# Performance work log

Measured on AMD Instinct MI355X. Metric: run time of the kernel, lower is better.

The kernel has to match this reference:

```python
import jax, jax.numpy as jnp
import numpy as np

N_NODES = 100000
N_EDGES = 1600000
D_FEAT = 128
HIDDEN = 256


def setup_inputs() -> dict:
    key = jax.random.key(0)
    k1, k2, k3, k4, k5, k6, k7 = jax.random.split(key, 7)
    h = jax.random.normal(k1, (N_NODES, D_FEAT), dtype=jnp.float32)
    src = jax.random.randint(k2, (N_EDGES,), 0, N_NODES, dtype=jnp.int64)
    dst = jax.random.randint(k3, (N_EDGES,), 0, N_NODES, dtype=jnp.int64)
    # Linear weights, torch layout: W [out, in], b [out]
    lim1 = 1.0 / np.sqrt(2 * D_FEAT)
    W1_w = jax.random.uniform(k4, (HIDDEN, 2 * D_FEAT), minval=-lim1, maxval=lim1, dtype=jnp.float32)
    W1_b = jax.random.uniform(k5, (HIDDEN,), minval=-lim1, maxval=lim1, dtype=jnp.float32)
    lim2 = 1.0 / np.sqrt(HIDDEN)
    W2_w = jax.random.uniform(k6, (1, HIDDEN), minval=-lim2, maxval=lim2, dtype=jnp.float32)
    W2_b = jax.random.uniform(k7, (1,), minval=-lim2, maxval=lim2, dtype=jnp.float32)
    return {"h": h, "src": src, "dst": dst, "W1_w": W1_w, "W1_b": W1_b, "W2_w": W2_w, "W2_b": W2_b}


def reference(h, src, dst, W1_w, W1_b, W2_w, W2_b):
    # gather per-edge src/dst node features and concat: [E, 2D]
    x = jnp.concatenate([h[src], h[dst]], axis=1)
    # Linear -> ReLU -> Linear, squeeze last dim -> [E]
    hid = jax.nn.relu(x @ W1_w.T + W1_b)          # [E, H]
    score = (hid @ W2_w.T + W2_b)[:, 0]           # [E]
    return score
```

## Files before the change

### kernel.cpp

```cpp
#include <hip/hip_runtime.h>


#define NNODES 100000
#define E_TOTAL 1600000
#define D 128
#define K2 256
#define H 256

typedef short bf16x8 __attribute__((ext_vector_type(8)));
typedef float f32x4 __attribute__((ext_vector_type(4)));
typedef const __attribute__((address_space(1))) unsigned short* gas_t;
typedef __attribute__((address_space(3))) unsigned short* las_t;

__device__ __forceinline__ unsigned short f2bf(float f) {
    unsigned u = __float_as_uint(f);
    u += 0x7fff + ((u >> 16) & 1);
    return (unsigned short)(u >> 16);
}
__device__ __forceinline__ float bf2f(unsigned short s) {
    return __uint_as_float((unsigned)s << 16);
}

__global__ void cvt_kernel(const float* __restrict__ h, const float* __restrict__ w1,
                           unsigned short* __restrict__ hbf, unsigned short* __restrict__ w1bf,
                           int n4h, int n4w) {
    int i = blockIdx.x * blockDim.x + threadIdx.x;
    const float* s; unsigned short* d; int j;
    if (i < n4h) { s = h; d = hbf; j = i; }
    else if (i < n4h + n4w) { s = w1; d = w1bf; j = i - n4h; }
    else return;
    float4 v = ((const float4*)s)[j];
    ushort4 o;
    o.x = f2bf(v.x); o.y = f2bf(v.y); o.z = f2bf(v.z); o.w = f2bf(v.w);
    ((ushort4*)d)[j] = o;
}

__global__ __launch_bounds__(256, 4) void u_gemm3(
    const unsigned short* __restrict__ hbf,
    const unsigned short* __restrict__ w1bf,
    const float* __restrict__ b1,
    unsigned short* __restrict__ Us,
    unsigned short* __restrict__ Ud)
{
    __shared__ __align__(16) unsigned short A[64 * 128];

    const int tid = threadIdx.x;
    const int wave = tid >> 6;
    const int lane = tid & 63;
    const int l15 = lane & 15;
    const int quad = lane >> 4;

    const int tile = blockIdx.x >> 2;
    const int half = (blockIdx.x >> 1) & 1;
    const int nh = blockIdx.x & 1;
    const int r0 = tile * 64;
    int rows = NNODES - r0; if (rows > 64) rows = 64;
    const int koff = half * 128;
    unsigned short* U = half ? Ud : Us;

#pragma unroll
    for (int it = 0; it < 4; ++it) {
        const int s = it * 256 + tid;
        const int r = s >> 4;
        const int p = s & 15;
        const int c = p ^ (r & 15);
        if (r < rows)
            __builtin_amdgcn_global_load_lds(
                (gas_t)(hbf + (size_t)(r0 + r) * D + c * 8),
                (las_t)(A + it * 2048 + wave * 512), 16, 0, 0);
    }

    bf16x8 B[4][2];
    float bias[2];
#pragma unroll
    for (int nt = 0; nt < 2; ++nt) {
        const int n = nh * 128 + wave * 32 + nt * 16 + l15;
        bias[nt] = half ? 0.f : b1[n];
#pragma unroll
        for (int kit = 0; kit < 4; ++kit)
            B[kit][nt] = *(const bf16x8*)(w1bf + (size_t)n * K2 + koff + kit * 32 + quad * 8);
    }

    __syncthreads();

    f32x4 acc[4][2];
    const f32x4 zero = {0.f, 0.f, 0.f, 0.f};
#pragma unroll
    for (int ms = 0; ms < 4; ++ms)
#pragma unroll
        for (int nt = 0; nt < 2; ++nt)
            acc[ms][nt] = zero;

#pragma unroll
    for (int kit = 0; kit < 4; ++kit) {
        bf16x8 a[4];
#pragma unroll
        for (int ms = 0; ms < 4; ++ms) {
            const int row = ms * 16 + l15;
            const int p = (kit * 4 + quad) ^ l15;
            a[ms] = *(const bf16x8*)&A[row * 128 + p * 8];
        }
#pragma unroll
        for (int ms = 0; ms < 4; ++ms)
#pragma unroll
            for (int nt = 0; nt < 2; ++nt)
                acc[ms][nt] = __builtin_amdgcn_mfma_f32_16x16x32_bf16(
                    a[ms], B[kit][nt], acc[ms][nt], 0, 0, 0);
    }

    const int coff = nh * 128 + wave * 32 + l15 * 2;
#pragma unroll
    for (int ms = 0; ms < 4; ++ms) {
#pragma unroll
        for (int r = 0; r < 4; ++r) {
            const int m = ms * 16 + quad * 4 + r;
            if (m < rows) {
                const unsigned lo = f2bf(acc[ms][0][r] + bias[0]);
                const unsigned hi = f2bf(acc[ms][1][r] + bias[1]);
                *(unsigned*)(U + (size_t)(r0 + m) * H + coff) = lo | (hi << 16);
            }
        }
    }
}

__global__ __launch_bounds__(256) void edge_score(
    const unsigned short* __restrict__ Us,
    const unsigned short* __restrict__ Ud,
    const int* __restrict__ srcE,
    const int* __restrict__ dstE,
    const float* __restrict__ w2,
    const float* __restrict__ b2p,
    float* __restrict__ out)
{
    const int gt = blockIdx.x * 256 + threadIdx.x;
    const int l = gt & 15;
    const int q = gt >> 4;
    const int Q = (gridDim.x * 256) >> 4;
    const int NGRP = E_TOTAL / 4;

    float w2v[16];
#pragma unroll
    for (int j = 0; j < 16; ++j) {
        const int cp = l * 16 + j;
        const int n = (cp & ~31) + ((cp & 1) << 4) + ((cp & 31) >> 1);
        w2v[j] = w2[n];
    }
    const float b2 = *b2p;

    for (int g = q; g < NGRP; g += Q) {
        const int e0 = g * 4;
        const int4 s4 = *(const int4*)(srcE + e0);
        const int4 d4 = *(const int4*)(dstE + e0);
        const int sv[4] = {s4.x, s4.y, s4.z, s4.w};
        const int dv[4] = {d4.x, d4.y, d4.z, d4.w};

        bf16x8 u[4][2], v[4][2];
#pragma unroll
        for (int k = 0; k < 4; ++k) {
            const bf16x8* us = (const bf16x8*)(Us + (size_t)sv[k] * H + l * 16);
            const bf16x8* ud = (const bf16x8*)(Ud + (size_t)dv[k] * H + l * 16);
            u[k][0] = us[0]; u[k][1] = us[1];
            v[k][0] = ud[0]; v[k][1] = ud[1];
        }

        float4 res;
        float* resp = (float*)&res;
#pragma unroll
        for (int k = 0; k < 4; ++k) {
            float acc = 0.f;
#pragma unroll
            for (int j = 0; j < 8; ++j) {
                float hv = bf2f((unsigned short)u[k][0][j]) + bf2f((unsigned short)v[k][0][j]);
                acc = fmaf(fmaxf(hv, 0.f), w2v[j], acc);
            }
#pragma unroll
            for (int j = 0; j < 8; ++j) {
                float hv = bf2f((unsigned short)u[k][1][j]) + bf2f((unsigned short)v[k][1][j]);
                acc = fmaf(fmaxf(hv, 0.f), w2v[j + 8], acc);
            }
            acc += __shfl_xor(acc, 1, 16);
            acc += __shfl_xor(acc, 2, 16);
            acc += __shfl_xor(acc, 4, 16);
            acc += __shfl_xor(acc, 8, 16);
            resp[k] = acc + b2;
        }
        if (l == 0) *(float4*)(out + e0) = res;
    }
}


#define TILE_M 32
#define NTILES (E_TOTAL / TILE_M)
#define GRID 2500

#if defined(__has_attribute)
#if __has_attribute(amdgpu_waves_per_eu)
#define LB __launch_bounds__(256) __attribute__((amdgpu_waves_per_eu(2, 2)))
#else
#define LB __launch_bounds__(256, 2)
#endif
#else
#define LB __launch_bounds__(256, 2)
#endif

__global__ LB void edge_mlp(
    const unsigned short* __restrict__ hbf,
    const int* __restrict__ srcE,
    const int* __restrict__ dstE,
    const unsigned short* __restrict__ w1bf,
    const float* __restrict__ b1,
    const float* __restrict__ w2,
    const float* __restrict__ b2p,
    float* __restrict__ out)
{
    __shared__ __align__(16) unsigned short X[2][TILE_M * K2];
    __shared__ float red[2][TILE_M][5];

    const int tid = threadIdx.x;
    const int wave = tid >> 6;
    const int lane = tid & 63;
    const int lane15 = lane & 15;
    const int quad = lane >> 4;

    bf16x8 B[8][4];
#pragma unroll
    for (int kit = 0; kit < 8; ++kit)
#pragma unroll
        for (int nt = 0; nt < 4; ++nt) {
            int n = wave * 64 + nt * 16 + lane15;
            int k = kit * 32 + quad * 8;
            B[kit][nt] = *(const bf16x8*)(w1bf + n * K2 + k);
        }

    float b1v[4], w2v[4];
#pragma unroll
    for (int nt = 0; nt < 4; ++nt) {
        int n = wave * 64 + nt * 16 + lane15;
        b1v[nt] = b1[n];
        w2v[nt] = w2[n];
    }
    const float b2 = *b2p;

    const int r_off = tid >> 5;
    const int c = (tid & 31) ^ (r_off & 7);
    const int half = c >> 4;
    const int fc = c & 15;
    const int* idx_base = half ? dstE : srcE;
    const int gshort = fc * 8;

    const int t0 = blockIdx.x;
    int inode[4];

#pragma unroll
    for (int it = 0; it < 4; ++it)
        inode[it] = idx_base[t0 * TILE_M + it * 8 + r_off];
#pragma unroll
    for (int it = 0; it < 4; ++it)
        __builtin_amdgcn_global_load_lds(
            (gas_t)(hbf + inode[it] * D + gshort),
            (las_t)(&X[0][0] + it * 2048 + wave * 512), 16, 0, 0);
    {
        const int t1 = t0 + GRID;
#pragma unroll
        for (int it = 0; it < 4; ++it)
            inode[it] = idx_base[t1 * TILE_M + it * 8 + r_off];
    }

    int buf = 0;
    int prev_eb = -1;

    for (int tile = t0; tile < NTILES; tile += GRID) {
        __syncthreads();

        const int nt1 = tile + GRID;
        if (nt1 < NTILES) {
            unsigned short* Xn = &X[buf ^ 1][0];
#pragma unroll
            for (int it = 0; it < 4; ++it)
                __builtin_amdgcn_global_load_lds(
                    (gas_t)(hbf + inode[it] * D + gshort),
                    (las_t)(Xn + it * 2048 + wave * 512), 16, 0, 0);
        }
        const int nt2 = tile + 2 * GRID;
        if (nt2 < NTILES) {
            const int eb2 = nt2 * TILE_M;
#pragma unroll
            for (int it = 0; it < 4; ++it)
                inode[it] = idx_base[eb2 + it * 8 + r_off];
        }
        if (prev_eb >= 0 && tid < TILE_M) {
            float s = b2;
#pragma unroll
            for (int w = 0; w < 4; ++w) s += red[buf ^ 1][tid][w];
            out[prev_eb + tid] = s;
        }

        const unsigned short* Xc = &X[buf][0];
        f32x4 acc[2][4];
        const f32x4 zero = {0.f, 0.f, 0.f, 0.f};
#pragma unroll
        for (int ms = 0; ms < 2; ++ms)
#pragma unroll
            for (int nt = 0; nt < 4; ++nt)
                acc[ms][nt] = zero;

#pragma unroll
        for (int kit = 0; kit < 8; ++kit) {
            const int p8 = (((kit * 4 + quad) ^ (lane15 & 7))) * 8;
            bf16x8 a[2];
#pragma unroll
            for (int ms = 0; ms < 2; ++ms)
                a[ms] = *(const bf16x8*)&Xc[(ms * 16 + lane15) * K2 + p8];
#pragma unroll
            for (int ms = 0; ms < 2; ++ms)
#pragma unroll
                for (int nt = 0; nt < 4; ++nt)
                    acc[ms][nt] = __builtin_amdgcn_mfma_f32_16x16x32_bf16(
                        a[ms], B[kit][nt], acc[ms][nt], 0, 0, 0);
        }

#pragma unroll
        for (int ms = 0; ms < 2; ++ms)
#pragma unroll
            for (int r = 0; r < 4; ++r) {
                float p = 0.f;
#pragma unroll
                for (int nt = 0; nt < 4; ++nt) {
                    float hv = acc[ms][nt][r] + b1v[nt];
                    p = fmaf(fmaxf(hv, 0.f), w2v[nt], p);
                }
                p += __shfl_xor(p, 1, 16);
                p += __shfl_xor(p, 2, 16);
                p += __shfl_xor(p, 4, 16);
                p += __shfl_xor(p, 8, 16);
                if (lane15 == 0) red[buf][ms * 16 + quad * 4 + r][wave] = p;
            }
        prev_eb = tile * TILE_M;
        buf ^= 1;
    }

    __syncthreads();
    if (prev_eb >= 0 && tid < TILE_M) {
        float s = b2;
#pragma unroll
        for (int w = 0; w < 4; ++w) s += red[buf ^ 1][tid][w];
        out[prev_eb + tid] = s;
    }
}


extern "C" void kernel_launch(void* const* d_in, const int* in_sizes, int n_in,
                              void* d_out, int out_size, void* d_ws, size_t ws_size,
                              hipStream_t stream) {
    const float* h    = (const float*)d_in[0];
    const int*   srcE = (const int*)d_in[1];
    const int*   dstE = (const int*)d_in[2];
    const float* W1   = (const float*)d_in[3];
    const float* b1   = (const float*)d_in[4];
    const float* w2   = (const float*)d_in[5];
    const float* b2   = (const float*)d_in[6];
    float* out = (float*)d_out;

    char* ws = (char*)d_ws;
    const size_t offUs   = 0;
    const size_t offUd   = 51200000;
    const size_t offHbf  = 102400000;
    const size_t offW1bf = 128000000;
    const size_t need    = offW1bf + 131072;

    if (ws_size >= need) {
        unsigned short* Us   = (unsigned short*)(ws + offUs);
        unsigned short* Ud   = (unsigned short*)(ws + offUd);
        unsigned short* hbf  = (unsigned short*)(ws + offHbf);
        unsigned short* w1bf = (unsigned short*)(ws + offW1bf);

        int n4h = NNODES * D / 4, n4w = H * K2 / 4;
        cvt_kernel<<<(n4h + n4w + 255) / 256, 256, 0, stream>>>(h, W1, hbf, w1bf, n4h, n4w);
        u_gemm3<<<4 * ((NNODES + 63) / 64), 256, 0, stream>>>(hbf, w1bf, b1, Us, Ud);
        edge_score<<<4096, 256, 0, stream>>>(Us, Ud, srcE, dstE, w2, b2, out);
    } else {
        unsigned short* hbf  = (unsigned short*)d_ws;
        unsigned short* w1bf = hbf + (size_t)NNODES * D;
        int n4h = NNODES * D / 4, n4w = H * K2 / 4;
        cvt_kernel<<<(n4h + n4w + 255) / 256, 256, 0, stream>>>(h, W1, hbf, w1bf, n4h, n4w);
        edge_mlp<<<GRID, 256, 0, stream>>>(hbf, srcE, dstE, w1bf, b1, w2, b2, out);
    }
}
```

Measured before the change: 359.7 us.

## Split edge scoring into two half-hidden passes to shrink gathered working set

The edge-scoring kernel now runs twice, each pass gathering only 128 of the 256 hidden columns from the per-node Us/Ud tables. The second pass reads back and accumulates the partial result written by the first. The intent is to halve the random-gather footprint per pass so more of each half-table stays resident in cache. In exchange it adds an extra launch, a second read of the edge index arrays, and a read-modify-write of the output.

```diff
diff --git a/kernel.cpp b/kernel.cpp
--- a/kernel.cpp
+++ b/kernel.cpp
@@ -123,14 +123,15 @@
     }
 }
 
-__global__ __launch_bounds__(256) void edge_score(
+__global__ __launch_bounds__(256) void edge_score_half(
     const unsigned short* __restrict__ Us,
     const unsigned short* __restrict__ Ud,
     const int* __restrict__ srcE,
     const int* __restrict__ dstE,
     const float* __restrict__ w2,
     const float* __restrict__ b2p,
-    float* __restrict__ out)
+    float* __restrict__ out,
+    int half)
 {
     const int gt = blockIdx.x * 256 + threadIdx.x;
     const int l = gt & 15;
@@ -138,14 +139,15 @@
     const int Q = (gridDim.x * 256) >> 4;
     const int NGRP = E_TOTAL / 4;
 
-    float w2v[16];
-#pragma unroll
-    for (int j = 0; j < 16; ++j) {
-        const int cp = l * 16 + j;
+    float w2v[8];
+#pragma unroll
+    for (int j = 0; j < 8; ++j) {
+        const int cp = half * 128 + l * 8 + j;
         const int n = (cp & ~31) + ((cp & 1) << 4) + ((cp & 31) >> 1);
         w2v[j] = w2[n];
     }
     const float b2 = *b2p;
+    const int loff = half * 128 + l * 8;
 
     for (int g = q; g < NGRP; g += Q) {
         const int e0 = g * 4;
@@ -154,35 +156,32 @@
         const int sv[4] = {s4.x, s4.y, s4.z, s4.w};
         const int dv[4] = {d4.x, d4.y, d4.z, d4.w};
 
-        bf16x8 u[4][2], v[4][2];
+        bf16x8 u[4], v[4];
 #pragma unroll
         for (int k = 0; k < 4; ++k) {
-            const bf16x8* us = (const bf16x8*)(Us + (size_t)sv[k] * H + l * 16);
-            const bf16x8* ud = (const bf16x8*)(Ud + (size_t)dv[k] * H + l * 16);
-            u[k][0] = us[0]; u[k][1] = us[1];
-            v[k][0] = ud[0]; v[k][1] = ud[1];
-        }
+            u[k] = *(const bf16x8*)(Us + (size_t)sv[k] * H + loff);
+            v[k] = *(const bf16x8*)(Ud + (size_t)dv[k] * H + loff);
+        }
+
+        float4 prev;
+        if (half) prev = *(const float4*)(out + e0);
 
         float4 res;
         float* resp = (float*)&res;
+        const float* prevp = (const float*)&prev;
 #pragma unroll
         for (int k = 0; k < 4; ++k) {
             float acc = 0.f;
 #pragma unroll
             for (int j = 0; j < 8; ++j) {
-                float hv = bf2f((unsigned short)u[k][0][j]) + bf2f((unsigned short)v[k][0][j]);
+                float hv = bf2f((unsigned short)u[k][j]) + bf2f((unsigned short)v[k][j]);
                 acc = fmaf(fmaxf(hv, 0.f), w2v[j], acc);
-            }
-#pragma unroll
-            for (int j = 0; j < 8; ++j) {
-                float hv = bf2f((unsigned short)u[k][1][j]) + bf2f((unsigned short)v[k][1][j]);
-                acc = fmaf(fmaxf(hv, 0.f), w2v[j + 8], acc);
             }
             acc += __shfl_xor(acc, 1, 16);
             acc += __shfl_xor(acc, 2, 16);
             acc += __shfl_xor(acc, 4, 16);
             acc += __shfl_xor(acc, 8, 16);
-            resp[k] = acc + b2;
+            resp[k] = acc + (half ? prevp[k] : b2);
         }
         if (l == 0) *(float4*)(out + e0) = res;
     }
@@ -377,7 +376,8 @@
         int n4h = NNODES * D / 4, n4w = H * K2 / 4;
         cvt_kernel<<<(n4h + n4w + 255) / 256, 256, 0, stream>>>(h, W1, hbf, w1bf, n4h, n4w);
         u_gemm3<<<4 * ((NNODES + 63) / 64), 256, 0, stream>>>(hbf, w1bf, b1, Us, Ud);
-        edge_score<<<4096, 256, 0, stream>>>(Us, Ud, srcE, dstE, w2, b2, out);
+        edge_score_half<<<4096, 256, 0, stream>>>(Us, Ud, srcE, dstE, w2, b2, out, 0);
+        edge_score_half<<<4096, 256, 0, stream>>>(Us, Ud, srcE, dstE, w2, b2, out, 1);
     } else {
         unsigned short* hbf  = (unsigned short*)d_ws;
         unsigned short* w1bf = hbf + (size_t)NNODES * D;
```

Result: no change. 363.7 us (+1.1%).

## Bucket-sort edges by source node block before per-edge gather scoring

Applied to the files above, without the earlier changes.

Adds a counting sort of edges into 64-node source buckets: the histogram is fused into the GEMM kernel, followed by a single-block scan and an atomic scatter. The scoring kernel then walks the sorted edges, so Us rows are gathered with better locality, and it writes each result back to the edge's original index. XCD-aware block remapping is also applied to both the GEMM and the scoring grid to improve L2 locality per chiplet. The cost is two extra launches, atomic scatter traffic, extra index arrays and scattered output writes.

```diff
diff --git a/kernel.cpp b/kernel.cpp
--- a/kernel.cpp
+++ b/kernel.cpp
@@ -6,6 +6,8 @@
 #define D 128
 #define K2 256
 #define H 256
+#define NBUCK ((NNODES + 63) >> 6)
+#define EDGE_GRID 3125
 
 typedef short bf16x8 __attribute__((ext_vector_type(8)));
 typedef float f32x4 __attribute__((ext_vector_type(4)));
@@ -21,14 +23,24 @@
     return __uint_as_float((unsigned)s << 16);
 }
 
+__device__ __forceinline__ int xcd_chunk(int orig, int nwg) {
+    const int q = nwg >> 3, r = nwg & 7;
+    const int x = orig & 7, s = orig >> 3;
+    return (x < r ? x * (q + 1) : r * (q + 1) + (x - r) * q) + s;
+}
+
 __global__ void cvt_kernel(const float* __restrict__ h, const float* __restrict__ w1,
                            unsigned short* __restrict__ hbf, unsigned short* __restrict__ w1bf,
-                           int n4h, int n4w) {
+                           int n4h, int n4w, int* __restrict__ hist, int nz) {
     int i = blockIdx.x * blockDim.x + threadIdx.x;
+    if (i >= n4h + n4w) {
+        int z = i - (n4h + n4w);
+        if (z < nz) hist[z] = 0;
+        return;
+    }
     const float* s; unsigned short* d; int j;
     if (i < n4h) { s = h; d = hbf; j = i; }
-    else if (i < n4h + n4w) { s = w1; d = w1bf; j = i - n4h; }
-    else return;
+    else { s = w1; d = w1bf; j = i - n4h; }
     float4 v = ((const float4*)s)[j];
     ushort4 o;
     o.x = f2bf(v.x); o.y = f2bf(v.y); o.z = f2bf(v.z); o.w = f2bf(v.w);
@@ -40,7 +52,9 @@
     const unsigned short* __restrict__ w1bf,
     const float* __restrict__ b1,
     unsigned short* __restrict__ Us,
-    unsigned short* __restrict__ Ud)
+    unsigned short* __restrict__ Ud,
+    const int* __restrict__ srcE,
+    int* __restrict__ hist)
 {
     __shared__ __align__(16) unsigned short A[64 * 128];
 
@@ -50,9 +64,10 @@
     const int l15 = lane & 15;
     const int quad = lane >> 4;
 
-    const int tile = blockIdx.x >> 2;
-    const int half = (blockIdx.x >> 1) & 1;
-    const int nh = blockIdx.x & 1;
+    const int L = xcd_chunk(blockIdx.x, gridDim.x);
+    const int tile = L >> 2;
+    const int half = (L >> 1) & 1;
+    const int nh = L & 1;
     const int r0 = tile * 64;
     int rows = NNODES - r0; if (rows > 64) rows = 64;
     const int koff = half * 128;
@@ -70,6 +85,11 @@
                 (las_t)(A + it * 2048 + wave * 512), 16, 0, 0);
     }
 
+    if (hist) {
+        const int gid = blockIdx.x * 256 + tid;
+        if (gid < E_TOTAL) atomicAdd(&hist[srcE[gid] >> 6], 1);
+    }
+
     bf16x8 B[4][2];
     float bias[2];
 #pragma unroll
@@ -119,6 +139,117 @@
                 const unsigned hi = f2bf(acc[ms][1][r] + bias[1]);
                 *(unsigned*)(U + (size_t)(r0 + m) * H + coff) = lo | (hi << 16);
             }
+        }
+    }
+}
+
+__global__ void scan_kernel(const int* __restrict__ hist, int* __restrict__ cursor) {
+    __shared__ int tsum[256];
+    const int t = threadIdx.x;
+    int loc[7];
+    int s = 0;
+#pragma unroll
+    for (int j = 0; j < 7; ++j) {
+        const int idx = t * 7 + j;
+        const int v = (idx < NBUCK) ? hist[idx] : 0;
+        loc[j] = s; s += v;
+    }
+    tsum[t] = s;
+    __syncthreads();
+    for (int off = 1; off < 256; off <<= 1) {
+        const int v = (t >= off) ? tsum[t - off] : 0;
+        __syncthreads();
+        tsum[t] += v;
+        __syncthreads();
+    }
+    const int excl = tsum[t] - s;
+#pragma unroll
+    for (int j = 0; j < 7; ++j) {
+        const int idx = t * 7 + j;
+        if (idx < NBUCK) cursor[idx] = excl + loc[j];
+    }
+}
+
+__global__ __launch_bounds__(256) void scatter_kernel(
+    const int* __restrict__ srcE, const int* __restrict__ dstE,
+    int* __restrict__ cursor,
+    int* __restrict__ ss, int* __restrict__ sd, int* __restrict__ si)
+{
+    const int e = blockIdx.x * 256 + threadIdx.x;
+    const int s = srcE[e];
+    const int d = dstE[e];
+    const int p = atomicAdd(&cursor[s >> 6], 1);
+    ss[p] = s; sd[p] = d; si[p] = e;
+}
+
+__global__ __launch_bounds__(256) void edge_score_sorted(
+    const unsigned short* __restrict__ Us,
+    const unsigned short* __restrict__ Ud,
+    const int* __restrict__ ss,
+    const int* __restrict__ sd,
+    const int* __restrict__ si,
+    const float* __restrict__ w2,
+    const float* __restrict__ b2p,
+    float* __restrict__ out)
+{
+    const int b = xcd_chunk(blockIdx.x, gridDim.x);
+    const int tid = threadIdx.x;
+    const int l = tid & 15;
+    const int grp = b * 16 + (tid >> 4);
+
+    float w2v[16];
+#pragma unroll
+    for (int j = 0; j < 16; ++j) {
+        const int cp = l * 16 + j;
+        const int n = (cp & ~31) + ((cp & 1) << 4) + ((cp & 31) >> 1);
+        w2v[j] = w2[n];
+    }
+    const float b2 = *b2p;
+
+    const int g0 = grp * 8;
+    for (int g = g0; g < g0 + 8; ++g) {
+        const int e0 = g * 4;
+        const int4 s4 = *(const int4*)(ss + e0);
+        const int4 d4 = *(const int4*)(sd + e0);
+        const int4 i4 = *(const int4*)(si + e0);
+        const int sv[4] = {s4.x, s4.y, s4.z, s4.w};
+        const int dv[4] = {d4.x, d4.y, d4.z, d4.w};
+
+        bf16x8 u[4][2], v[4][2];
+#pragma unroll
+        for (int k = 0; k < 4; ++k) {
+            const bf16x8* us = (const bf16x8*)(Us + (size_t)sv[k] * H + l * 16);
+            const bf16x8* ud = (const bf16x8*)(Ud + (size_t)dv[k] * H + l * 16);
+            u[k][0] = us[0]; u[k][1] = us[1];
+            v[k][0] = ud[0]; v[k][1] = ud[1];
+        }
+
+        float4 res;
+        float* resp = (float*)&res;
+#pragma unroll
+        for (int k = 0; k < 4; ++k) {
+            float acc = 0.f;
+#pragma unroll
+            for (int j = 0; j < 8; ++j) {
+                float hv = bf2f((unsigned short)u[k][0][j]) + bf2f((unsigned short)v[k][0][j]);
+                acc = fmaf(fmaxf(hv, 0.f), w2v[j], acc);
+            }
+#pragma unroll
+            for (int j = 0; j < 8; ++j) {
+                float hv = bf2f((unsigned short)u[k][1][j]) + bf2f((unsigned short)v[k][1][j]);
+                acc = fmaf(fmaxf(hv, 0.f), w2v[j + 8], acc);
+            }
+            acc += __shfl_xor(acc, 1, 16);
+            acc += __shfl_xor(acc, 2, 16);
+            acc += __shfl_xor(acc, 4, 16);
+            acc += __shfl_xor(acc, 8, 16);
+            resp[k] = acc + b2;
+        }
+        if (l == 0) {
+            out[i4.x] = res.x;
+            out[i4.y] = res.y;
+            out[i4.z] = res.z;
+            out[i4.w] = res.w;
         }
     }
 }
@@ -367,22 +498,44 @@
     const size_t offHbf  = 102400000;
     const size_t offW1bf = 128000000;
     const size_t need    = offW1bf + 131072;
+    const size_t offHist = need;
+    const size_t offCur  = offHist + 8192;
+    const size_t offSS   = offCur + 8192;
+    const size_t offSD   = offSS + 6400000;
+    const size_t offSI   = offSD + 6400000;
+    const size_t need2   = offSI + 6400000;
 
     if (ws_size >= need) {
         unsigned short* Us   = (unsigned short*)(ws + offUs);
         unsigned short* Ud   = (unsigned short*)(ws + offUd);
         unsigned short* hbf  = (unsigned short*)(ws + offHbf);
         unsigned short* w1bf = (unsigned short*)(ws + offW1bf);
+        const bool sorted = (ws_size >= need2);
+        int* hist = sorted ? (int*)(ws + offHist) : (int*)nullptr;
+        int* cur  = (int*)(ws + offCur);
+        int* ss   = (int*)(ws + offSS);
+        int* sd   = (int*)(ws + offSD);
+        int* si   = (int*)(ws + offSI);
 
         int n4h = NNODES * D / 4, n4w = H * K2 / 4;
-        cvt_kernel<<<(n4h + n4w + 255) / 256, 256, 0, stream>>>(h, W1, hbf, w1bf, n4h, n4w);
-        u_gemm3<<<4 * ((NNODES + 63) / 64), 256, 0, stream>>>(hbf, w1bf, b1, Us, Ud);
-        edge_score<<<4096, 256, 0, stream>>>(Us, Ud, srcE, dstE, w2, b2, out);
+        const int nz = sorted ? NBUCK : 0;
+        cvt_kernel<<<(n4h + n4w + nz + 255) / 256, 256, 0, stream>>>(
+            h, W1, hbf, w1bf, n4h, n4w, hist, nz);
+        u_gemm3<<<4 * ((NNODES + 63) / 64), 256, 0, stream>>>(
+            hbf, w1bf, b1, Us, Ud, srcE, hist);
+        if (sorted) {
+            scan_kernel<<<1, 256, 0, stream>>>(hist, cur);
+            scatter_kernel<<<E_TOTAL / 256, 256, 0, stream>>>(srcE, dstE, cur, ss, sd, si);
+            edge_score_sorted<<<EDGE_GRID, 256, 0, stream>>>(Us, Ud, ss, sd, si, w2, b2, out);
+        } else {
+            edge_score<<<4096, 256, 0, stream>>>(Us, Ud, srcE, dstE, w2, b2, out);
+        }
     } else {
         unsigned short* hbf  = (unsigned short*)d_ws;
         unsigned short* w1bf = hbf + (size_t)NNODES * D;
         int n4h = NNODES * D / 4, n4w = H * K2 / 4;
-        cvt_kernel<<<(n4h + n4w + 255) / 256, 256, 0, stream>>>(h, W1, hbf, w1bf, n4h, n4w);
+        cvt_kernel<<<(n4h + n4w + 255) / 256, 256, 0, stream>>>(
+            h, W1, hbf, w1bf, n4h, n4w, nullptr, 0);
         edge_mlp<<<GRID, 256, 0, stream>>>(hbf, srcE, dstE, w1bf, b1, w2, b2, out);
     }
 }
```

New measurement: 771.4 us. +114.5%, slower.
